# Kernel optimization log

Measured on AMD Instinct MI355X. Metric: run time of the kernel, lower is better.

The kernel has to match this reference:

```python
import jax, jax.numpy as jnp
import numpy as np

ALPHA = 0.25
GAMMA = 2.0


def setup_inputs() -> dict:
    key = jax.random.key(0)
    k1, k2, k3, k4, k5, k6, k7, k8 = jax.random.split(key, 8)
    B, A, C, M = 8, 120000, 80, 32
    # sigmoid-ed class probabilities in (0,1)
    classifications = jax.random.uniform(k1, (B, A, C), jnp.float32, 1e-4, 1.0 - 1e-4)
    regressions = jax.random.normal(k2, (B, A, 4), jnp.float32) * 0.1
    # anchors in [y1, x1, y2, x2] (widths = a[:,3]-a[:,1] in original code)
    cx = jax.random.uniform(k3, (A,), jnp.float32, 0.0, 800.0)
    cy = jax.random.uniform(k4, (A,), jnp.float32, 0.0, 800.0)
    wh = jax.random.uniform(k5, (A, 2), jnp.float32, 16.0, 256.0)  # (w, h)
    anchors = jnp.stack([cy - 0.5 * wh[:, 1], cx - 0.5 * wh[:, 0],
                         cy + 0.5 * wh[:, 1], cx + 0.5 * wh[:, 0]], axis=1)[None]  # [1,A,4]
    # annotations per image: [x1, y1, x2, y2, class]
    xy1 = jax.random.uniform(k6, (B, M, 2), jnp.float32, 0.0, 600.0)
    bwh = jax.random.uniform(k7, (B, M, 2), jnp.float32, 20.0, 200.0)
    cls_ids = jax.random.randint(k8, (B, M, 1), 0, C).astype(jnp.float32)
    annotations = jnp.concatenate([xy1, xy1 + bwh, cls_ids], axis=2)
    return dict(classifications=classifications, regressions=regressions,
                anchors=anchors, annotations=annotations)


def _calc_iou(a, b):
    # a: anchors [A,4] in [y1,x1,y2,x2]; b: gt boxes [M,4] in [x1,y1,x2,y2]
    m = jnp.max(a)
    a = a / m
    b = b / m
    area = (b[:, 2] - b[:, 0]) * (b[:, 3] - b[:, 1])                 # [M]
    iw = jnp.minimum(a[:, 3:4], b[:, 2]) - jnp.maximum(a[:, 1:2], b[:, 0])  # [A,M]
    ih = jnp.minimum(a[:, 2:3], b[:, 3]) - jnp.maximum(a[:, 0:1], b[:, 1])
    iw = jnp.maximum(iw, 0.0)
    ih = jnp.maximum(ih, 0.0)
    ua = ((a[:, 2] - a[:, 0]) * (a[:, 3] - a[:, 1]))[:, None] + area - iw * ih
    ua = jnp.maximum(ua, 1e-8)
    return iw * ih / ua                                              # [A,M]


def _giou_loss(pred, gt):
    # pred, gt: [A,4] in [x1,y1,x2,y2]
    px1 = jnp.minimum(pred[:, 0], pred[:, 2]); py1 = jnp.minimum(pred[:, 1], pred[:, 3])
    px2 = jnp.maximum(pred[:, 0], pred[:, 2]); py2 = jnp.maximum(pred[:, 1], pred[:, 3])
    gx1 = jnp.minimum(gt[:, 0], gt[:, 2]);     gy1 = jnp.minimum(gt[:, 1], gt[:, 3])
    gx2 = jnp.maximum(gt[:, 0], gt[:, 2]);     gy2 = jnp.maximum(gt[:, 1], gt[:, 3])
    iw = jnp.maximum(jnp.minimum(px2, gx2) - jnp.maximum(px1, gx1), 0.0)
    ih = jnp.maximum(jnp.minimum(py2, gy2) - jnp.maximum(py1, gy1), 0.0)
    inter = iw * ih
    area_p = jnp.maximum((px2 - px1) * (py2 - py1), 1e-6)
    area_g = jnp.maximum((gx2 - gx1) * (gy2 - gy1), 1e-6)
    union = area_p + area_g - inter
    iou = inter / (union + 1e-7)
    wc = jnp.maximum(jnp.maximum(px2, gx2) - jnp.minimum(px1, gx1), 1e-6)
    hc = jnp.maximum(jnp.maximum(py2, gy2) - jnp.minimum(py1, gy1), 1e-6)
    area_c = wc * hc
    giou = jnp.clip(iou - (area_c - union) / (area_c + 1e-7), -1.0, 1.0)
    return 1.0 - giou


def _reorder(b):
    return jnp.stack([jnp.minimum(b[:, 0], b[:, 2]), jnp.minimum(b[:, 1], b[:, 3]),
                      jnp.maximum(b[:, 0], b[:, 2]), jnp.maximum(b[:, 1], b[:, 3])], axis=1)


def reference(classifications, regressions, anchors, annotations):
    anchor = anchors[0]                                   # [A,4] (y1,x1,y2,x2)
    aw = anchor[:, 3] - anchor[:, 1]
    ah = anchor[:, 2] - anchor[:, 0]
    acx = anchor[:, 1] + 0.5 * aw
    acy = anchor[:, 0] + 0.5 * ah
    C = classifications.shape[-1]

    def per_image(cls, reg, ann):
        cls = jnp.clip(cls, 0.0005, 1.0 - 0.0005)          # [A,C]
        iou = _calc_iou(anchor, ann[:, :4])                # [A,M]
        iou_max = jnp.max(iou, axis=1)
        iou_arg = jnp.argmax(iou, axis=1)
        assigned = ann[iou_arg]                            # [A,5]
        pos = iou_max >= 0.5                               # [A]
        t = jnp.full_like(cls, -1.0)
        t = jnp.where((iou_max < 0.4)[:, None], 0.0, t)
        onehot = jax.nn.one_hot(assigned[:, 4].astype(jnp.int32), C, dtype=cls.dtype)
        t = jnp.where(pos[:, None], onehot, t)
        alpha_factor = jnp.where(t == 1.0, ALPHA, 1.0 - ALPHA)
        focal_w = alpha_factor * jnp.where(t == 1.0, 1.0 - cls, cls) ** GAMMA
        bce = -(t * jnp.log(cls) + (1.0 - t) * jnp.log(1.0 - cls))
        cls_loss = jnp.where(t != -1.0, focal_w * bce, 0.0)
        npos = jnp.sum(pos).astype(cls.dtype)
        c_loss = jnp.sum(cls_loss) / jnp.maximum(npos, 1.0)
        # decode predicted boxes for ALL anchors (mask positives in the reduction)
        ty, tx, th, tw = reg[:, 0], reg[:, 1], reg[:, 2], reg[:, 3]
        pcx = tx * aw + acx
        pcy = ty * ah + acy
        pw = jnp.exp(tw) * aw
        ph = jnp.exp(th) * ah
        pred = jnp.stack([pcx - 0.5 * pw, pcy - 0.5 * ph,
                          pcx + 0.5 * pw, pcy + 0.5 * ph], axis=1)
        pred = jnp.maximum(pred, 0.0)
        gt = jnp.maximum(assigned[:, :4], 0.0)
        giou = _giou_loss(_reorder(pred), _reorder(gt))    # [A]
        r_loss = jnp.where(npos > 0,
                           jnp.sum(giou * pos.astype(cls.dtype)) / jnp.maximum(npos, 1.0),
                           0.0)
        return c_loss, r_loss

    c, r = jax.vmap(per_image)(classifications, regressions, annotations)
    c_loss = jnp.mean(c)
    r_loss = jnp.mean(r)
    return c_loss + r_loss, c_loss, r_loss
```

## Files before the change

### kernel.cpp

```cpp
#include <hip/hip_runtime.h>

#define B_IMG 8
#define A_TOTAL 120000
#define C_CLS 80
#define M_ANN 32
#define APB 256
#define THREADS 256
#define NBLK_X 469
#define NBLK   (NBLK_X * B_IMG)
#define NEG075LN2 (-0.51986038542f)

__global__ __launch_bounds__(THREADS) void focal_main_kernel(
    const float* __restrict__ cls,
    const float* __restrict__ reg,
    const float* __restrict__ anchors,
    const float* __restrict__ ann,
    float* __restrict__ ws)
{
    __shared__ float m_s[APB];
    __shared__ float red_c[4], red_r[4], red_n[4];

    const int b   = blockIdx.y;
    const int a0  = blockIdx.x * APB;
    const int tid = threadIdx.x;
    const int nA  = min(APB, A_TOTAL - a0);
    const float* __restrict__ annb = ann + b * (M_ANN * 5);

    float r_acc = 0.0f, n_acc = 0.0f, c_acc = 0.0f;
    float mval  = 0.0f;
    const bool full = (nA == APB);

    const float4* __restrict__ cp =
        (const float4*)(cls + ((size_t)b * A_TOTAL + a0) * C_CLS);

    float4 v0, v1, v2, v3, v4, v5, v6, v7, v8, v9;
    if (full) {
        v0 = cp[tid];
        v1 = cp[tid + 256];
        v2 = cp[tid + 512];
        v3 = cp[tid + 768];
        v4 = cp[tid + 1024];
        v5 = cp[tid + 1280];
        v6 = cp[tid + 1536];
        v7 = cp[tid + 1792];
        v8 = cp[tid + 2048];
        v9 = cp[tid + 2304];
    }

    if (tid < nA) {
        const int a = a0 + tid;
        float4 anc = ((const float4*)anchors)[a];
        float ay1 = anc.x, ax1 = anc.y, ay2 = anc.z, ax2 = anc.w;
        float area_a = (ay2 - ay1) * (ax2 - ax1);
        float binter = 0.0f, bua = 1.0f;
        int   barg = 0;
        #pragma unroll
        for (int j = 0; j < M_ANN; ++j) {
            float bx1 = annb[j * 5 + 0], by1 = annb[j * 5 + 1];
            float bx2 = annb[j * 5 + 2], by2 = annb[j * 5 + 3];
            float iw = fmaxf(fminf(ax2, bx2) - fmaxf(ax1, bx1), 0.0f);
            float ih = fmaxf(fminf(ay2, by2) - fmaxf(ay1, by1), 0.0f);
            float inter = iw * ih;
            float ua = fmaxf(area_a + (bx2 - bx1) * (by2 - by1) - inter, 1e-8f);
            bool gt = inter * bua > binter * ua;
            binter = gt ? inter : binter;
            bua    = gt ? ua    : bua;
            barg   = gt ? j     : barg;
        }
        bool pos = binter >= 0.5f * bua;
        bool neg = binter <  0.4f * bua;
        mval = (pos || neg) ? NEG075LN2 : 0.0f;

        if (pos) {
            n_acc = 1.0f;
            int k = (int)annb[barg * 5 + 4];
            float cv = cls[((size_t)b * A_TOTAL + a) * C_CLS + k];
            float c  = fminf(fmaxf(cv, 5e-4f), 1.0f - 5e-4f);
            float omc = 1.0f - c;
            c_acc += 0.25f * omc * omc * (-__logf(c))
                   - 0.75f * c * c * (-__logf(omc));

            float4 rg = ((const float4*)reg)[(size_t)b * A_TOTAL + a];
            float ty = rg.x, tx = rg.y, th = rg.z, tw = rg.w;
            float aw = ax2 - ax1, ah = ay2 - ay1;
            float acx = ax1 + 0.5f * aw, acy = ay1 + 0.5f * ah;
            float pcx = tx * aw + acx, pcy = ty * ah + acy;
            float pw = __expf(tw) * aw, ph = __expf(th) * ah;
            float px1 = fmaxf(pcx - 0.5f * pw, 0.0f);
            float py1 = fmaxf(pcy - 0.5f * ph, 0.0f);
            float px2 = fmaxf(pcx + 0.5f * pw, 0.0f);
            float py2 = fmaxf(pcy + 0.5f * ph, 0.0f);
            float gx1 = fmaxf(annb[barg * 5 + 0], 0.0f);
            float gy1 = fmaxf(annb[barg * 5 + 1], 0.0f);
            float gx2 = fmaxf(annb[barg * 5 + 2], 0.0f);
            float gy2 = fmaxf(annb[barg * 5 + 3], 0.0f);
            float iw2 = fmaxf(fminf(px2, gx2) - fmaxf(px1, gx1), 0.0f);
            float ih2 = fmaxf(fminf(py2, gy2) - fmaxf(py1, gy1), 0.0f);
            float inter2 = iw2 * ih2;
            float area_p = fmaxf((px2 - px1) * (py2 - py1), 1e-6f);
            float area_g = fmaxf((gx2 - gx1) * (gy2 - gy1), 1e-6f);
            float uni = area_p + area_g - inter2;
            float iou2 = inter2 / (uni + 1e-7f);
            float wc = fmaxf(fmaxf(px2, gx2) - fminf(px1, gx1), 1e-6f);
            float hc = fmaxf(fmaxf(py2, gy2) - fminf(py1, gy1), 1e-6f);
            float area_c = wc * hc;
            float giou = fminf(fmaxf(iou2 - (area_c - uni) / (area_c + 1e-7f), -1.0f), 1.0f);
            r_acc = 1.0f - giou;
        }
    }
    m_s[tid] = (tid < nA) ? mval : 0.0f;
    __syncthreads();

#define FOCAL4(v, idx)                                                    \
    {                                                                     \
        float m_ = m_s[(unsigned)(idx) / 20u];                            \
        float s_, c_;                                                     \
        c_ = fminf(fmaxf((v).x, 5e-4f), 1.0f - 5e-4f);                    \
        s_ = c_ * c_ * __log2f(1.0f - c_);                                \
        c_ = fminf(fmaxf((v).y, 5e-4f), 1.0f - 5e-4f);                    \
        s_ = fmaf(c_ * c_, __log2f(1.0f - c_), s_);                       \
        c_ = fminf(fmaxf((v).z, 5e-4f), 1.0f - 5e-4f);                    \
        s_ = fmaf(c_ * c_, __log2f(1.0f - c_), s_);                       \
        c_ = fminf(fmaxf((v).w, 5e-4f), 1.0f - 5e-4f);                    \
        s_ = fmaf(c_ * c_, __log2f(1.0f - c_), s_);                       \
        c_acc = fmaf(m_, s_, c_acc);                                      \
    }

    if (full) {
        FOCAL4(v0, tid)
        FOCAL4(v1, tid + 256)
        FOCAL4(v2, tid + 512)
        FOCAL4(v3, tid + 768)
        FOCAL4(v4, tid + 1024)
        FOCAL4(v5, tid + 1280)
        FOCAL4(v6, tid + 1536)
        FOCAL4(v7, tid + 1792)
        FOCAL4(v8, tid + 2048)
        FOCAL4(v9, tid + 2304)
        const int base = tid + 2560;
        v0 = cp[base];
        v1 = cp[base + 256];
        v2 = cp[base + 512];
        v3 = cp[base + 768];
        v4 = cp[base + 1024];
        v5 = cp[base + 1280];
        v6 = cp[base + 1536];
        v7 = cp[base + 1792];
        v8 = cp[base + 2048];
        v9 = cp[base + 2304];
        FOCAL4(v0, base)
        FOCAL4(v1, base + 256)
        FOCAL4(v2, base + 512)
        FOCAL4(v3, base + 768)
        FOCAL4(v4, base + 1024)
        FOCAL4(v5, base + 1280)
        FOCAL4(v6, base + 1536)
        FOCAL4(v7, base + 1792)
        FOCAL4(v8, base + 2048)
        FOCAL4(v9, base + 2304)
    } else {
        const int nf4 = nA * (C_CLS / 4);
        for (int i = tid; i < nf4; i += THREADS) {
            float4 v = cp[i];
            FOCAL4(v, i)
        }
    }
#undef FOCAL4

    #pragma unroll
    for (int o = 32; o > 0; o >>= 1) {
        c_acc += __shfl_down(c_acc, o);
        r_acc += __shfl_down(r_acc, o);
        n_acc += __shfl_down(n_acc, o);
    }
    int wid = tid >> 6;
    if ((tid & 63) == 0) { red_c[wid] = c_acc; red_r[wid] = r_acc; red_n[wid] = n_acc; }
    __syncthreads();
    if (tid == 0) {
        const int slot = b * NBLK_X + blockIdx.x;
        ws[slot]            = red_c[0] + red_c[1] + red_c[2] + red_c[3];
        ws[NBLK + slot]     = red_r[0] + red_r[1] + red_r[2] + red_r[3];
        ws[2 * NBLK + slot] = red_n[0] + red_n[1] + red_n[2] + red_n[3];
    }
}

__global__ __launch_bounds__(THREADS) void finalize_kernel(
    const float* __restrict__ ws, float* __restrict__ out)
{
    __shared__ float sc[B_IMG], sr[B_IMG], sn[B_IMG];
    const int tid    = threadIdx.x;
    const int img    = tid >> 5;
    const int lane32 = tid & 31;

    float pc = 0.0f, pr = 0.0f, pn = 0.0f;
    for (int i = lane32; i < NBLK_X; i += 32) {
        const int slot = img * NBLK_X + i;
        pc += ws[slot];
        pr += ws[NBLK + slot];
        pn += ws[2 * NBLK + slot];
    }
    #pragma unroll
    for (int o = 16; o > 0; o >>= 1) {
        pc += __shfl_down(pc, o, 32);
        pr += __shfl_down(pr, o, 32);
        pn += __shfl_down(pn, o, 32);
    }
    if (lane32 == 0) { sc[img] = pc; sr[img] = pr; sn[img] = pn; }
    __syncthreads();
    if (tid == 0) {
        float c_tot = 0.0f, r_tot = 0.0f;
        #pragma unroll
        for (int b = 0; b < B_IMG; ++b) {
            float ns = sn[b];
            c_tot += sc[b] / fmaxf(ns, 1.0f);
            r_tot += (ns > 0.0f) ? (sr[b] / fmaxf(ns, 1.0f)) : 0.0f;
        }
        c_tot *= (1.0f / B_IMG);
        r_tot *= (1.0f / B_IMG);
        out[0] = c_tot + r_tot;
        out[1] = c_tot;
        out[2] = r_tot;
    }
}

extern "C" void kernel_launch(void* const* d_in, const int* in_sizes, int n_in,
                              void* d_out, int out_size, void* d_ws, size_t ws_size,
                              hipStream_t stream) {
    const float* cls     = (const float*)d_in[0];
    const float* reg     = (const float*)d_in[1];
    const float* anchors = (const float*)d_in[2];
    const float* ann     = (const float*)d_in[3];
    float* ws  = (float*)d_ws;
    float* out = (float*)d_out;

    dim3 grid(NBLK_X, B_IMG);
    hipLaunchKernelGGL(focal_main_kernel, grid, dim3(THREADS), 0, stream,
                       cls, reg, anchors, ann, ws);
    hipLaunchKernelGGL(finalize_kernel, dim3(1), dim3(THREADS), 0, stream, ws, out);
}
```

Measured before the change: 68.85 us.

## Convert focal loss kernel to persistent blocks overlapping IoU with class streaming

After: 84.65 us. 23.0% more time.

```diff
diff --git a/kernel.cpp b/kernel.cpp
--- a/kernel.cpp
+++ b/kernel.cpp
@@ -6,49 +6,23 @@
 #define M_ANN 32
 #define APB 256
 #define THREADS 256
-#define NBLK_X 469
-#define NBLK   (NBLK_X * B_IMG)
+#define IPB 128
+#define NTILE 469
+#define TAIL_T 468
+#define TAIL_NA 192
+#define NSLOT (IPB * B_IMG)
 #define NEG075LN2 (-0.51986038542f)
 
-__global__ __launch_bounds__(THREADS) void focal_main_kernel(
-    const float* __restrict__ cls,
-    const float* __restrict__ reg,
-    const float* __restrict__ anchors,
-    const float* __restrict__ ann,
-    float* __restrict__ ws)
+
+__device__ __forceinline__ void phase1_tile(
+    int b, int a0t, int nA, int tid,
+    const float* __restrict__ cls, const float* __restrict__ reg,
+    const float* __restrict__ anchors, const float* __restrict__ annb,
+    float& mval, float& c_acc, float& r_acc, float& n_acc)
 {
-    __shared__ float m_s[APB];
-    __shared__ float red_c[4], red_r[4], red_n[4];
-
-    const int b   = blockIdx.y;
-    const int a0  = blockIdx.x * APB;
-    const int tid = threadIdx.x;
-    const int nA  = min(APB, A_TOTAL - a0);
-    const float* __restrict__ annb = ann + b * (M_ANN * 5);
-
-    float r_acc = 0.0f, n_acc = 0.0f, c_acc = 0.0f;
-    float mval  = 0.0f;
-    const bool full = (nA == APB);
-
-    const float4* __restrict__ cp =
-        (const float4*)(cls + ((size_t)b * A_TOTAL + a0) * C_CLS);
-
-    float4 v0, v1, v2, v3, v4, v5, v6, v7, v8, v9;
-    if (full) {
-        v0 = cp[tid];
-        v1 = cp[tid + 256];
-        v2 = cp[tid + 512];
-        v3 = cp[tid + 768];
-        v4 = cp[tid + 1024];
-        v5 = cp[tid + 1280];
-        v6 = cp[tid + 1536];
-        v7 = cp[tid + 1792];
-        v8 = cp[tid + 2048];
-        v9 = cp[tid + 2304];
-    }
-
+    mval = 0.0f;
     if (tid < nA) {
-        const int a = a0 + tid;
+        const int a = a0t + tid;
         float4 anc = ((const float4*)anchors)[a];
         float ay1 = anc.x, ax1 = anc.y, ay2 = anc.z, ax2 = anc.w;
         float area_a = (ay2 - ay1) * (ax2 - ax1);
@@ -72,7 +46,7 @@
         mval = (pos || neg) ? NEG075LN2 : 0.0f;
 
         if (pos) {
-            n_acc = 1.0f;
+            n_acc += 1.0f;
             int k = (int)annb[barg * 5 + 4];
             float cv = cls[((size_t)b * A_TOTAL + a) * C_CLS + k];
             float c  = fminf(fmaxf(cv, 5e-4f), 1.0f - 5e-4f);
@@ -105,15 +79,44 @@
             float hc = fmaxf(fmaxf(py2, gy2) - fminf(py1, gy1), 1e-6f);
             float area_c = wc * hc;
             float giou = fminf(fmaxf(iou2 - (area_c - uni) / (area_c + 1e-7f), -1.0f), 1.0f);
-            r_acc = 1.0f - giou;
-        }
-    }
-    m_s[tid] = (tid < nA) ? mval : 0.0f;
+            r_acc += 1.0f - giou;
+        }
+    }
+}
+
+__global__ __launch_bounds__(THREADS, 4) void focal_persist_kernel(
+    const float* __restrict__ cls,
+    const float* __restrict__ reg,
+    const float* __restrict__ anchors,
+    const float* __restrict__ ann,
+    float* __restrict__ ws)
+{
+    __shared__ float m_s[APB];
+    __shared__ float red_c[4], red_r[4], red_n[4];
+
+    const int b   = blockIdx.y;
+    const int k   = blockIdx.x;
+    const int tid = threadIdx.x;
+    const float* __restrict__ annb = ann + b * (M_ANN * 5);
+    const int nt = (k <= (NTILE - 1 - 3 * IPB)) ? 4 : 3;
+
+    float c_acc = 0.0f, r_acc = 0.0f, n_acc = 0.0f;
+
+    {
+        float mval;
+        const int t0 = k;
+        phase1_tile(b, t0 * APB, (t0 == TAIL_T) ? TAIL_NA : APB, tid,
+                    cls, reg, anchors, annb, mval, c_acc, r_acc, n_acc);
+        m_s[tid] = mval;
+    }
     __syncthreads();
 
-#define FOCAL4(v, idx)                                                    \
+    const float4* __restrict__ cpimg =
+        (const float4*)(cls + (size_t)b * A_TOTAL * C_CLS);
+
+#define FOCAL4(v, l)                                                      \
     {                                                                     \
-        float m_ = m_s[(unsigned)(idx) / 20u];                            \
+        float m_ = m_s[(unsigned)(l) / 20u];                              \
         float s_, c_;                                                     \
         c_ = fminf(fmaxf((v).x, 5e-4f), 1.0f - 5e-4f);                    \
         s_ = c_ * c_ * __log2f(1.0f - c_);                                \
@@ -126,43 +129,71 @@
         c_acc = fmaf(m_, s_, c_acc);                                      \
     }
 
-    if (full) {
-        FOCAL4(v0, tid)
-        FOCAL4(v1, tid + 256)
-        FOCAL4(v2, tid + 512)
-        FOCAL4(v3, tid + 768)
-        FOCAL4(v4, tid + 1024)
-        FOCAL4(v5, tid + 1280)
-        FOCAL4(v6, tid + 1536)
-        FOCAL4(v7, tid + 1792)
-        FOCAL4(v8, tid + 2048)
-        FOCAL4(v9, tid + 2304)
-        const int base = tid + 2560;
-        v0 = cp[base];
-        v1 = cp[base + 256];
-        v2 = cp[base + 512];
-        v3 = cp[base + 768];
-        v4 = cp[base + 1024];
-        v5 = cp[base + 1280];
-        v6 = cp[base + 1536];
-        v7 = cp[base + 1792];
-        v8 = cp[base + 2048];
-        v9 = cp[base + 2304];
-        FOCAL4(v0, base)
-        FOCAL4(v1, base + 256)
-        FOCAL4(v2, base + 512)
-        FOCAL4(v3, base + 768)
-        FOCAL4(v4, base + 1024)
-        FOCAL4(v5, base + 1280)
-        FOCAL4(v6, base + 1536)
-        FOCAL4(v7, base + 1792)
-        FOCAL4(v8, base + 2048)
-        FOCAL4(v9, base + 2304)
-    } else {
-        const int nf4 = nA * (C_CLS / 4);
-        for (int i = tid; i < nf4; i += THREADS) {
-            float4 v = cp[i];
-            FOCAL4(v, i)
+    for (int i = 0; i < nt; ++i) {
+        const int t = k + i * IPB;
+        float mnext = 0.0f;
+        const bool have_next = (i + 1 < nt);
+
+        if (t != TAIL_T) {
+            const float4* __restrict__ cp = cpimg + (size_t)t * (APB * 20);
+            float4 v0 = cp[tid];
+            float4 v1 = cp[tid + 256];
+            float4 v2 = cp[tid + 512];
+            float4 v3 = cp[tid + 768];
+            float4 v4 = cp[tid + 1024];
+            float4 v5 = cp[tid + 1280];
+            float4 v6 = cp[tid + 1536];
+            float4 v7 = cp[tid + 1792];
+            float4 v8 = cp[tid + 2048];
+            float4 v9 = cp[tid + 2304];
+            if (have_next) {
+                const int tn = t + IPB;
+                phase1_tile(b, tn * APB, (tn == TAIL_T) ? TAIL_NA : APB, tid,
+                            cls, reg, anchors, annb, mnext, c_acc, r_acc, n_acc);
+            }
+            FOCAL4(v0, tid)
+            FOCAL4(v1, tid + 256)
+            FOCAL4(v2, tid + 512)
+            FOCAL4(v3, tid + 768)
+            FOCAL4(v4, tid + 1024)
+            FOCAL4(v5, tid + 1280)
+            FOCAL4(v6, tid + 1536)
+            FOCAL4(v7, tid + 1792)
+            FOCAL4(v8, tid + 2048)
+            FOCAL4(v9, tid + 2304)
+            const int base = tid + 2560;
+            v0 = cp[base];
+            v1 = cp[base + 256];
+            v2 = cp[base + 512];
+            v3 = cp[base + 768];
+            v4 = cp[base + 1024];
+            v5 = cp[base + 1280];
+            v6 = cp[base + 1536];
+            v7 = cp[base + 1792];
+            v8 = cp[base + 2048];
+            v9 = cp[base + 2304];
+            FOCAL4(v0, base)
+            FOCAL4(v1, base + 256)
+            FOCAL4(v2, base + 512)
+            FOCAL4(v3, base + 768)
+            FOCAL4(v4, base + 1024)
+            FOCAL4(v5, base + 1280)
+            FOCAL4(v6, base + 1536)
+            FOCAL4(v7, base + 1792)
+            FOCAL4(v8, base + 2048)
+            FOCAL4(v9, base + 2304)
+        } else {
+            const float4* __restrict__ cp = cpimg + (size_t)t * (APB * 20);
+            for (int l = tid; l < TAIL_NA * 20; l += THREADS) {
+                float4 v = cp[l];
+                FOCAL4(v, l)
+            }
+        }
+
+        if (have_next) {
+            __syncthreads();
+            m_s[tid] = mnext;
+            __syncthreads();
         }
     }
 #undef FOCAL4
@@ -177,10 +208,10 @@
     if ((tid & 63) == 0) { red_c[wid] = c_acc; red_r[wid] = r_acc; red_n[wid] = n_acc; }
     __syncthreads();
     if (tid == 0) {
-        const int slot = b * NBLK_X + blockIdx.x;
-        ws[slot]            = red_c[0] + red_c[1] + red_c[2] + red_c[3];
-        ws[NBLK + slot]     = red_r[0] + red_r[1] + red_r[2] + red_r[3];
-        ws[2 * NBLK + slot] = red_n[0] + red_n[1] + red_n[2] + red_n[3];
+        const int slot = b * IPB + k;
+        ws[slot]             = red_c[0] + red_c[1] + red_c[2] + red_c[3];
+        ws[NSLOT + slot]     = red_r[0] + red_r[1] + red_r[2] + red_r[3];
+        ws[2 * NSLOT + slot] = red_n[0] + red_n[1] + red_n[2] + red_n[3];
     }
 }
 
@@ -193,11 +224,11 @@
     const int lane32 = tid & 31;
 
     float pc = 0.0f, pr = 0.0f, pn = 0.0f;
-    for (int i = lane32; i < NBLK_X; i += 32) {
-        const int slot = img * NBLK_X + i;
+    for (int i = lane32; i < IPB; i += 32) {
+        const int slot = img * IPB + i;
         pc += ws[slot];
-        pr += ws[NBLK + slot];
-        pn += ws[2 * NBLK + slot];
+        pr += ws[NSLOT + slot];
+        pn += ws[2 * NSLOT + slot];
     }
     #pragma unroll
     for (int o = 16; o > 0; o >>= 1) {
@@ -233,8 +264,8 @@
     float* ws  = (float*)d_ws;
     float* out = (float*)d_out;
 
-    dim3 grid(NBLK_X, B_IMG);
-    hipLaunchKernelGGL(focal_main_kernel, grid, dim3(THREADS), 0, stream,
+    dim3 grid(IPB, B_IMG);
+    hipLaunchKernelGGL(focal_persist_kernel, grid, dim3(THREADS), 0, stream,
                        cls, reg, anchors, ann, ws);
     hipLaunchKernelGGL(finalize_kernel, dim3(1), dim3(THREADS), 0, stream, ws, out);
 }
```
